# Kernel tuning notes

Hardware: AMD Instinct MI355X
Metric: run time of the kernel (lower is better)

Reference implementation:

```python
import jax, jax.numpy as jnp
import numpy as np

N = 4096      # num_nodes (also node feature dim)
E = 32768     # num_edges
EMB = 8       # embedding_dim


def setup_inputs() -> dict:
    key = jax.random.key(0)
    ks = jax.random.split(key, 12)
    s = lambda fan_in: 1.0 / np.sqrt(fan_in)
    return {
        "x": jax.random.normal(ks[0], (N, N), dtype=jnp.float32),
        "edge_index": jax.random.randint(ks[1], (2, E), 0, N, dtype=jnp.int64),
        "edge_weight": jax.random.uniform(ks[2], (E,), dtype=jnp.float32),
        # GCNConv linear (PyG Linear, weight [out,in]) + bias
        "gcn_w": jax.random.normal(ks[3], (N, N), dtype=jnp.float32) * s(N),
        "gcn_b": jnp.zeros((N,), dtype=jnp.float32),
        # Wq: Linear(N -> E)
        "wq_w": jax.random.normal(ks[4], (E, N), dtype=jnp.float32) * s(N),
        "wq_b": jax.random.normal(ks[5], (E,), dtype=jnp.float32) * s(N),
        # edge embedding table [E, EMB]
        "emb": jax.random.normal(ks[6], (E, EMB), dtype=jnp.float32),
        # WF: Linear(N+EMB -> 1)
        "wf_w": jax.random.normal(ks[7], (1, N + EMB), dtype=jnp.float32) * s(N + EMB),
        "wf_b": jax.random.normal(ks[8], (1,), dtype=jnp.float32) * s(N + EMB),
    }


def reference(x, edge_index, edge_weight, gcn_w, gcn_b, wq_w, wq_b, emb, wf_w, wf_b):
    n = x.shape[0]
    row, col = edge_index[0], edge_index[1]
    # --- GCNConv: add self loops (weight 1.0), symmetric normalization ---
    loop = jnp.arange(n)
    row_f = jnp.concatenate([row, loop])
    col_f = jnp.concatenate([col, loop])
    w_f = jnp.concatenate([edge_weight, jnp.ones((n,), dtype=x.dtype)])
    deg = jax.ops.segment_sum(w_f, col_f, num_segments=n)          # weighted in-degree
    dis = jnp.where(deg > 0, jax.lax.rsqrt(deg), 0.0)              # deg^{-1/2}, 0 for isolated
    norm = dis[row_f] * w_f * dis[col_f]                           # [E+N]
    h = x @ gcn_w.T                                                # linear transform first (as PyG)
    agg = jax.ops.segment_sum(norm[:, None] * h[row_f], col_f, num_segments=n)
    H1 = jnp.tanh(agg + gcn_b)                                     # [N, N]
    # --- dense head ---
    H2 = jnp.tanh(H1 @ wq_w.T + wq_b)                              # [N, E]
    H2_t = H2.T                                                    # [E, N]
    feat = jnp.concatenate([H2_t, emb], axis=1)                    # [E, N+EMB]
    F_hat = (feat @ wf_w.T + wf_b)[:, 0]                           # [E]
    return F_hat
```

## Files before the change

kernel.cpp:

```cpp
#include <hip/hip_runtime.h>
#include <hip/hip_bf16.h>

#define NN 4096
#define NE 32768
#define NEMB 8

typedef __bf16 bf16x8 __attribute__((ext_vector_type(8)));
typedef float  f32x4  __attribute__((ext_vector_type(4)));

__device__ __forceinline__ unsigned short f2bf(float f) {
  union { float f; unsigned int u; } v; v.f = f;
  return (unsigned short)((v.u + 0x7FFFu + ((v.u >> 16) & 1u)) >> 16);
}

__global__ void k_f2bf(const float* __restrict__ in, unsigned short* __restrict__ out, long n8) {
  long i = (long)blockIdx.x * blockDim.x + threadIdx.x;
  long stride = (long)gridDim.x * blockDim.x;
  for (long j = i; j < n8; j += stride) {
    const float* p = in + j * 8;
    float4 a = *(const float4*)p;
    float4 b = *(const float4*)(p + 4);
    union { unsigned short u[8]; uint4 v; } o;
    o.u[0] = f2bf(a.x); o.u[1] = f2bf(a.y); o.u[2] = f2bf(a.z); o.u[3] = f2bf(a.w);
    o.u[4] = f2bf(b.x); o.u[5] = f2bf(b.y); o.u[6] = f2bf(b.z); o.u[7] = f2bf(b.w);
    *(uint4*)(out + j * 8) = o.v;
  }
}

__global__ void k_deg_init(float* deg) { deg[blockIdx.x * 256 + threadIdx.x] = 1.0f; }

__global__ void k_edge_accum(const int* __restrict__ ei, const float* __restrict__ ew,
                             float* deg, int* cnt) {
  int e = blockIdx.x * 256 + threadIdx.x;
  if (e >= NE) return;
  int c = ei[NE + e];
  atomicAdd(&deg[c], ew[e]);
  atomicAdd(&cnt[c], 1);
}

__global__ void k_dis(const float* __restrict__ deg, float* __restrict__ dis) {
  int i = blockIdx.x * 256 + threadIdx.x;
  float d = deg[i];
  dis[i] = d > 0.f ? rsqrtf(d) : 0.f;
}

__global__ void k_scan(const int* __restrict__ cnt, int* __restrict__ starts) {
  __shared__ int sh[1024];
  int tid = threadIdx.x;
  int base = tid * 4;
  int v[4]; int sum = 0;
  for (int i = 0; i < 4; i++) { v[i] = cnt[base + i]; sum += v[i]; }
  sh[tid] = sum;
  __syncthreads();
  for (int offd = 1; offd < 1024; offd <<= 1) {
    int t = (tid >= offd) ? sh[tid - offd] : 0;
    __syncthreads();
    sh[tid] += t;
    __syncthreads();
  }
  int run = sh[tid] - sum;
  for (int i = 0; i < 4; i++) { starts[base + i] = run; run += v[i]; }
}

__global__ void k_fill(const int* __restrict__ ei, const int* __restrict__ starts,
                       int* cursor, int* csr_e) {
  int e = blockIdx.x * 256 + threadIdx.x;
  if (e >= NE) return;
  int c = ei[NE + e];
  int pos = atomicAdd(&cursor[c], 1);
  csr_e[starts[c] + pos] = e;
}

__global__ void k_sortnorm(const int* __restrict__ ei, const float* __restrict__ ew,
                           const int* __restrict__ starts, const int* __restrict__ cnt,
                           const float* __restrict__ dis,
                           int* csr_e, int* __restrict__ csr_row, float* __restrict__ csr_nrm) {
  int n = blockIdx.x * 256 + threadIdx.x;
  if (n >= NN) return;
  int s = starts[n], c = cnt[n];
  for (int i = 1; i < c; i++) {
    int key = csr_e[s + i]; int j = i - 1;
    while (j >= 0 && csr_e[s + j] > key) { csr_e[s + j + 1] = csr_e[s + j]; j--; }
    csr_e[s + j + 1] = key;
  }
  float dn = dis[n];
  for (int i = 0; i < c; i++) {
    int e = csr_e[s + i];
    int r = ei[e];
    csr_row[s + i] = r;
    csr_nrm[s + i] = dis[r] * ew[e] * dn;
  }
}

__global__ __launch_bounds__(256) void k_agg(
    const float* __restrict__ h, const float* __restrict__ dis,
    const int* __restrict__ starts, const int* __restrict__ cnt,
    const int* __restrict__ csr_row, const float* __restrict__ csr_nrm,
    const float* __restrict__ gcn_b, unsigned short* __restrict__ H1b) {
  int n = blockIdx.x;
  int tid = threadIdx.x;
  float dn = dis[n];
  float sw = dn * dn;
  float acc[16];
  const float* hn = h + (size_t)n * NN;
  #pragma unroll
  for (int i = 0; i < 16; i++) { int f = tid + i * 256; acc[i] = sw * hn[f] + gcn_b[f]; }
  int s = starts[n], c = cnt[n];
  __shared__ int   s_row[64];
  __shared__ float s_nrm[64];
  for (int base = 0; base < c; base += 64) {
    int m = min(64, c - base);
    __syncthreads();
    if (tid < m) { s_row[tid] = csr_row[s + base + tid]; s_nrm[tid] = csr_nrm[s + base + tid]; }
    __syncthreads();
    for (int j = 0; j < m; j++) {
      const float* hr = h + (size_t)s_row[j] * NN;
      float wgt = s_nrm[j];
      #pragma unroll
      for (int i = 0; i < 16; i++) acc[i] += wgt * hr[tid + i * 256];
    }
  }
  #pragma unroll
  for (int i = 0; i < 16; i++)
    H1b[(size_t)n * NN + tid + i * 256] = f2bf(tanhf(acc[i]));
}

__device__ __forceinline__ void gload16(const void* g, void* l) {
  __builtin_amdgcn_global_load_lds(
      (const __attribute__((address_space(1))) unsigned int*)g,
      (__attribute__((address_space(3))) unsigned int*)l, 16, 0, 0);
}

#define BARX() do { __builtin_amdgcn_sched_barrier(0); __builtin_amdgcn_s_barrier(); __builtin_amdgcn_sched_barrier(0); } while (0)
#define VMC(n) do { asm volatile("s_waitcnt vmcnt(" #n ")" ::: "memory"); } while (0)


#define STAGE(buf, mat, kk, tk) do { \
    size_t off_ = (size_t)(tk) * 64 + (kk) * 32; \
    gload16((mat ? gB0 : gA0) + off_, &LDS[buf][mat][kk][c0][0]); \
    gload16((mat ? gB1 : gA1) + off_, &LDS[buf][mat][kk][c0 + 1][0]); \
  } while (0)

#define LDA4(dst, buf, kk, q) do { \
    const unsigned short* b_ = &LDS[buf][0][kk][wr * 8 + (q) * 4][0] + aoff; \
    dst[0] = *(const bf16x8*)(b_); \
    dst[1] = *(const bf16x8*)(b_ + 512); \
    dst[2] = *(const bf16x8*)(b_ + 1024); \
    dst[3] = *(const bf16x8*)(b_ + 1536); \
  } while (0)

#define LDB4(dst, buf, kk) do { \
    const unsigned short* b_ = &LDS[buf][1][kk][wc * 4][0] + aoff; \
    dst[0] = *(const bf16x8*)(b_); \
    dst[1] = *(const bf16x8*)(b_ + 512); \
    dst[2] = *(const bf16x8*)(b_ + 1024); \
    dst[3] = *(const bf16x8*)(b_ + 1536); \
  } while (0)

#define MMA16(q, av, bv) do { \
    __builtin_amdgcn_s_setprio(1); \
    _Pragma("unroll") \
    for (int mf_ = 0; mf_ < 4; mf_++) \
      _Pragma("unroll") \
      for (int nf_ = 0; nf_ < 4; nf_++) \
        acc[(q) * 4 + mf_][nf_] = __builtin_amdgcn_mfma_f32_16x16x32_bf16(av[mf_], bv[nf_], acc[(q) * 4 + mf_][nf_], 0, 0, 0); \
    __builtin_amdgcn_s_setprio(0); \
  } while (0)

template<bool FUSED>
__global__ __launch_bounds__(512, 2) void gemm8(
    const unsigned short* __restrict__ A,
    const unsigned short* __restrict__ B,
    int N, int K, int nRb,
    float* __restrict__ outF,
    const float* __restrict__ colBias,
    const float* __restrict__ rowW,
    float* __restrict__ P) {
  __shared__ unsigned short LDS[2][2][2][16][512];

  const int nwg = gridDim.x, n8 = nwg >> 3;
  const int bid = blockIdx.x;
  const int swz = (bid & 7) * n8 + (bid >> 3);
  const int rb = swz % nRb, cb = swz / nRb;
  const int row0 = rb * 256, col0 = cb * 256;

  const int tid = threadIdx.x;
  const int w = tid >> 6, l = tid & 63;
  const int wr = w >> 2, wc = w & 3;
  const int l15 = l & 15, kl = l >> 4;

  const int c0 = w * 2;
  const int pq = l >> 2;
  const int pc = (l & 3) ^ ((l >> 3) & 3);
  const unsigned short* gA0 = A + (size_t)(row0 + c0 * 16 + pq) * K + pc * 8;
  const unsigned short* gA1 = gA0 + (size_t)16 * K;
  const unsigned short* gB0 = B + (size_t)(col0 + c0 * 16 + pq) * K + pc * 8;
  const unsigned short* gB1 = gB0 + (size_t)16 * K;

  const int aoff = l15 * 32 + ((kl ^ ((l >> 1) & 3)) << 3);

  f32x4 acc[8][4];
  #pragma unroll
  for (int m = 0; m < 8; m++)
    #pragma unroll
    for (int n = 0; n < 4; n++)
      acc[m][n] = f32x4{0.f, 0.f, 0.f, 0.f};

  STAGE(0, 0, 0, 0); STAGE(0, 1, 0, 0); STAGE(0, 0, 1, 0); STAGE(0, 1, 1, 0);
  STAGE(1, 0, 0, 1); STAGE(1, 1, 0, 1);
  VMC(4);
  BARX();

  const int NIT = K >> 7;
  for (int i = 0; i < NIT; i++) {
    const int ta = 2 * i, tb = 2 * i + 1;
    const bool mid = (i < NIT - 1);
    bf16x8 av[4], bv[4];
    LDB4(bv, 0, 0); LDA4(av, 0, 0, 0);
    STAGE(1, 0, 1, tb);
    MMA16(0, av, bv);
    BARX();
    LDA4(av, 0, 0, 1);
    STAGE(1, 1, 1, tb);
    MMA16(1, av, bv);
    VMC(8);
    BARX();
    LDB4(bv, 0, 1); LDA4(av, 0, 1, 0);
    if (mid) STAGE(0, 0, 0, ta + 2);
    MMA16(0, av, bv);
    BARX();
    LDA4(av, 0, 1, 1);
    if (mid) STAGE(0, 1, 0, ta + 2);
    MMA16(1, av, bv);
    if (mid) VMC(8); else VMC(4);
    BARX();
    LDB4(bv, 1, 0); LDA4(av, 1, 0, 0);
    if (mid) STAGE(0, 0, 1, ta + 2);
    MMA16(0, av, bv);
    BARX();
    LDA4(av, 1, 0, 1);
    if (mid) STAGE(0, 1, 1, ta + 2);
    MMA16(1, av, bv);
    if (mid) VMC(8); else VMC(0);
    BARX();
    LDB4(bv, 1, 1); LDA4(av, 1, 1, 0);
    if (mid) STAGE(1, 0, 0, tb + 2);
    MMA16(0, av, bv);
    BARX();
    LDA4(av, 1, 1, 1);
    if (mid) STAGE(1, 1, 0, tb + 2);
    MMA16(1, av, bv);
    if (mid) VMC(8);
    BARX();
  }

  if (!FUSED) {
    #pragma unroll
    for (int mf = 0; mf < 8; mf++)
      #pragma unroll
      for (int nf = 0; nf < 4; nf++) {
        int row = row0 + wr * 128 + mf * 16 + kl * 4;
        int col = col0 + wc * 64 + nf * 16 + l15;
        float* o = outF + (size_t)row * N + col;
        #pragma unroll
        for (int r = 0; r < 4; r++) o[(size_t)r * N] = acc[mf][nf][r];
      }
  } else {
    #pragma unroll
    for (int nf = 0; nf < 4; nf++) {
      int col = col0 + wc * 64 + nf * 16 + l15;
      float bias = colBias[col];
      float s = 0.f;
      #pragma unroll
      for (int mf = 0; mf < 8; mf++) {
        int rbase = row0 + wr * 128 + mf * 16 + kl * 4;
        #pragma unroll
        for (int r = 0; r < 4; r++)
          s += rowW[rbase + r] * tanhf(acc[mf][nf][r] + bias);
      }
      s += __shfl_xor(s, 16, 64);
      s += __shfl_xor(s, 32, 64);
      if (l < 16) P[(size_t)(rb * 2 + wr) * N + col] = s;
    }
  }
}

__global__ void k_final(const float* __restrict__ P, const float* __restrict__ emb,
                        const float* __restrict__ wf, const float* __restrict__ wfb,
                        float* __restrict__ out) {
  int e = blockIdx.x * 256 + threadIdx.x;
  float s = 0.f;
  for (int r = 0; r < 32; r++) s += P[(size_t)r * NE + e];
  float c = wfb[0];
  #pragma unroll
  for (int k = 0; k < NEMB; k++) c += emb[e * NEMB + k] * wf[NN + k];
  out[e] = s + c;
}

extern "C" void kernel_launch(void* const* d_in, const int* in_sizes, int n_in,
                              void* d_out, int out_size, void* d_ws, size_t ws_size,
                              hipStream_t stream) {
  const float* x    = (const float*)d_in[0];
  const int*   ei   = (const int*)d_in[1];
  const float* ew   = (const float*)d_in[2];
  const float* gcnw = (const float*)d_in[3];
  const float* gcnb = (const float*)d_in[4];
  const float* wqw  = (const float*)d_in[5];
  const float* wqb  = (const float*)d_in[6];
  const float* emb  = (const float*)d_in[7];
  const float* wfw  = (const float*)d_in[8];
  const float* wfb  = (const float*)d_in[9];
  float* out = (float*)d_out;

  char* ws = (char*)d_ws;
  size_t off = 0;
  auto alloc = [&](size_t b) { char* p = ws + off; off += (b + 255) & ~(size_t)255; return p; };

  unsigned short* wq16  = (unsigned short*)alloc((size_t)NE * NN * 2);
  float*          h     = (float*)alloc((size_t)NN * NN * 4);
  unsigned short* x16   = (unsigned short*)alloc((size_t)NN * NN * 2);
  unsigned short* w16   = (unsigned short*)alloc((size_t)NN * NN * 2);
  unsigned short* h1b   = (unsigned short*)alloc((size_t)NN * NN * 2);
  float* deg    = (float*)alloc(NN * 4);
  float* dis    = (float*)alloc(NN * 4);
  int*   cnt    = (int*)alloc(NN * 4);
  int*   cursor = (int*)alloc(NN * 4);
  int*   starts = (int*)alloc(NN * 4);
  int*   csr_e  = (int*)alloc(NE * 4);
  int*   csr_row= (int*)alloc(NE * 4);
  float* csr_nrm= (float*)alloc(NE * 4);
  float* P      = (float*)alloc((size_t)32 * NE * 4);

  hipMemsetAsync(cnt, 0, NN * 4 * 2, stream);

  k_deg_init<<<NN / 256, 256, 0, stream>>>(deg);
  k_edge_accum<<<NE / 256, 256, 0, stream>>>(ei, ew, deg, cnt);
  k_dis<<<NN / 256, 256, 0, stream>>>(deg, dis);
  k_scan<<<1, 1024, 0, stream>>>(cnt, starts);
  k_fill<<<NE / 256, 256, 0, stream>>>(ei, starts, cursor, csr_e);
  k_sortnorm<<<NN / 256, 256, 0, stream>>>(ei, ew, starts, cnt, dis, csr_e, csr_row, csr_nrm);

  k_f2bf<<<1024, 256, 0, stream>>>(x, x16, (long)NN * NN / 8);
  k_f2bf<<<1024, 256, 0, stream>>>(gcnw, w16, (long)NN * NN / 8);
  k_f2bf<<<2048, 256, 0, stream>>>(wqw, wq16, (long)NE * NN / 8);

  gemm8<false><<<16 * 16, 512, 0, stream>>>(x16, w16, NN, NN, 16, h, nullptr, nullptr, nullptr);

  k_agg<<<NN, 256, 0, stream>>>(h, dis, starts, cnt, csr_row, csr_nrm, gcnb, h1b);

  gemm8<true><<<16 * 128, 512, 0, stream>>>(h1b, wq16, NE, NN, 16, nullptr, wqb, wfw, P);

  k_final<<<NE / 256, 256, 0, stream>>>(P, emb, wfw, wfb, out);
}
```

Measured before the change: 1.416 ms.

## Store GCN linear output as bf16 and interleave A-fragment LDS reads with MFMAs

The intermediate h = x @ gcn_w.T is now written and read as bf16 instead of fp32. This halves the store traffic of the first GEMM and the gather traffic in the aggregation kernel. The GEMM main loop is also restructured so the next A fragments are read from LDS inside the MFMA loop, software-pipelining LDS reads behind matrix ops, with a trailing MMA after the loop. The cost is reduced precision of h and more intricate register and barrier sequencing.

```diff
diff --git a/kernel.cpp b/kernel.cpp
--- a/kernel.cpp
+++ b/kernel.cpp
@@ -11,6 +11,10 @@
 __device__ __forceinline__ unsigned short f2bf(float f) {
   union { float f; unsigned int u; } v; v.f = f;
   return (unsigned short)((v.u + 0x7FFFu + ((v.u >> 16) & 1u)) >> 16);
+}
+__device__ __forceinline__ float b2f(unsigned short u) {
+  union { unsigned int u; float f; } v; v.u = ((unsigned int)u) << 16;
+  return v.f;
 }
 
 __global__ void k_f2bf(const float* __restrict__ in, unsigned short* __restrict__ out, long n8) {
@@ -93,7 +97,7 @@
 }
 
 __global__ __launch_bounds__(256) void k_agg(
-    const float* __restrict__ h, const float* __restrict__ dis,
+    const unsigned short* __restrict__ h, const float* __restrict__ dis,
     const int* __restrict__ starts, const int* __restrict__ cnt,
     const int* __restrict__ csr_row, const float* __restrict__ csr_nrm,
     const float* __restrict__ gcn_b, unsigned short* __restrict__ H1b) {
@@ -102,9 +106,9 @@
   float dn = dis[n];
   float sw = dn * dn;
   float acc[16];
-  const float* hn = h + (size_t)n * NN;
+  const unsigned short* hn = h + (size_t)n * NN;
   #pragma unroll
-  for (int i = 0; i < 16; i++) { int f = tid + i * 256; acc[i] = sw * hn[f] + gcn_b[f]; }
+  for (int i = 0; i < 16; i++) { int f = tid + i * 256; acc[i] = sw * b2f(hn[f]) + gcn_b[f]; }
   int s = starts[n], c = cnt[n];
   __shared__ int   s_row[64];
   __shared__ float s_nrm[64];
@@ -114,10 +118,10 @@
     if (tid < m) { s_row[tid] = csr_row[s + base + tid]; s_nrm[tid] = csr_nrm[s + base + tid]; }
     __syncthreads();
     for (int j = 0; j < m; j++) {
-      const float* hr = h + (size_t)s_row[j] * NN;
+      const unsigned short* hr = h + (size_t)s_row[j] * NN;
       float wgt = s_nrm[j];
       #pragma unroll
-      for (int i = 0; i < 16; i++) acc[i] += wgt * hr[tid + i * 256];
+      for (int i = 0; i < 16; i++) acc[i] += wgt * b2f(hr[tid + i * 256]);
     }
   }
   #pragma unroll
@@ -157,7 +161,20 @@
     dst[3] = *(const bf16x8*)(b_ + 1536); \
   } while (0)
 
-#define MMA16(q, av, bv) do { \
+#define MMA_RDA(q, bufA, kkA, qA) do { \
+    __builtin_amdgcn_s_setprio(1); \
+    _Pragma("unroll") \
+    for (int mf_ = 0; mf_ < 4; mf_++) { \
+      _Pragma("unroll") \
+      for (int nf_ = 0; nf_ < 4; nf_++) \
+        acc[(q) * 4 + mf_][nf_] = __builtin_amdgcn_mfma_f32_16x16x32_bf16(av[mf_], bv[nf_], acc[(q) * 4 + mf_][nf_], 0, 0, 0); \
+      const unsigned short* a_ = &LDS[bufA][0][kkA][wr * 8 + (qA) * 4 + mf_][0] + aoff; \
+      av[mf_] = *(const bf16x8*)(a_); \
+    } \
+    __builtin_amdgcn_s_setprio(0); \
+  } while (0)
+
+#define MMA16(q) do { \
     __builtin_amdgcn_s_setprio(1); \
     _Pragma("unroll") \
     for (int mf_ = 0; mf_ < 4; mf_++) \
@@ -172,7 +189,7 @@
     const unsigned short* __restrict__ A,
     const unsigned short* __restrict__ B,
     int N, int K, int nRb,
-    float* __restrict__ outF,
+    void* __restrict__ outP,
     const float* __restrict__ colBias,
     const float* __restrict__ rowW,
     float* __restrict__ P) {
@@ -206,6 +223,8 @@
     for (int n = 0; n < 4; n++)
       acc[m][n] = f32x4{0.f, 0.f, 0.f, 0.f};
 
+  bf16x8 av[4], bv[4];
+
   STAGE(0, 0, 0, 0); STAGE(0, 1, 0, 0); STAGE(0, 0, 1, 0); STAGE(0, 1, 1, 0);
   STAGE(1, 0, 0, 1); STAGE(1, 1, 0, 1);
   VMC(4);
@@ -215,55 +234,57 @@
   for (int i = 0; i < NIT; i++) {
     const int ta = 2 * i, tb = 2 * i + 1;
     const bool mid = (i < NIT - 1);
-    bf16x8 av[4], bv[4];
-    LDB4(bv, 0, 0); LDA4(av, 0, 0, 0);
+    if (i) {
+      MMA_RDA(1, 0, 0, 0);
+      LDB4(bv, 0, 0);
+    } else {
+      LDA4(av, 0, 0, 0);
+      LDB4(bv, 0, 0);
+    }
     STAGE(1, 0, 1, tb);
-    MMA16(0, av, bv);
-    BARX();
-    LDA4(av, 0, 0, 1);
+    BARX();
+    MMA_RDA(0, 0, 0, 1);
     STAGE(1, 1, 1, tb);
-    MMA16(1, av, bv);
     VMC(8);
     BARX();
-    LDB4(bv, 0, 1); LDA4(av, 0, 1, 0);
+    MMA_RDA(1, 0, 1, 0);
+    LDB4(bv, 0, 1);
     if (mid) STAGE(0, 0, 0, ta + 2);
-    MMA16(0, av, bv);
-    BARX();
-    LDA4(av, 0, 1, 1);
+    BARX();
+    MMA_RDA(0, 0, 1, 1);
     if (mid) STAGE(0, 1, 0, ta + 2);
-    MMA16(1, av, bv);
     if (mid) VMC(8); else VMC(4);
     BARX();
-    LDB4(bv, 1, 0); LDA4(av, 1, 0, 0);
+    MMA_RDA(1, 1, 0, 0);
+    LDB4(bv, 1, 0);
     if (mid) STAGE(0, 0, 1, ta + 2);
-    MMA16(0, av, bv);
-    BARX();
-    LDA4(av, 1, 0, 1);
+    BARX();
+    MMA_RDA(0, 1, 0, 1);
     if (mid) STAGE(0, 1, 1, ta + 2);
-    MMA16(1, av, bv);
     if (mid) VMC(8); else VMC(0);
     BARX();
-    LDB4(bv, 1, 1); LDA4(av, 1, 1, 0);
+    MMA_RDA(1, 1, 1, 0);
+    LDB4(bv, 1, 1);
     if (mid) STAGE(1, 0, 0, tb + 2);
-    MMA16(0, av, bv);
-    BARX();
-    LDA4(av, 1, 1, 1);
+    BARX();
+    MMA_RDA(0, 1, 1, 1);
     if (mid) STAGE(1, 1, 0, tb + 2);
-    MMA16(1, av, bv);
     if (mid) VMC(8);
     BARX();
   }
+  MMA16(1);
 
   if (!FUSED) {
+    unsigned short* outB = (unsigned short*)outP;
     #pragma unroll
     for (int mf = 0; mf < 8; mf++)
       #pragma unroll
       for (int nf = 0; nf < 4; nf++) {
         int row = row0 + wr * 128 + mf * 16 + kl * 4;
         int col = col0 + wc * 64 + nf * 16 + l15;
-        float* o = outF + (size_t)row * N + col;
+        unsigned short* o = outB + (size_t)row * N + col;
         #pragma unroll
-        for (int r = 0; r < 4; r++) o[(size_t)r * N] = acc[mf][nf][r];
+        for (int r = 0; r < 4; r++) o[(size_t)r * N] = f2bf(acc[mf][nf][r]);
       }
   } else {
     #pragma unroll
@@ -317,7 +338,7 @@
   auto alloc = [&](size_t b) { char* p = ws + off; off += (b + 255) & ~(size_t)255; return p; };
 
   unsigned short* wq16  = (unsigned short*)alloc((size_t)NE * NN * 2);
-  float*          h     = (float*)alloc((size_t)NN * NN * 4);
+  unsigned short* h     = (unsigned short*)alloc((size_t)NN * NN * 2);
   unsigned short* x16   = (unsigned short*)alloc((size_t)NN * NN * 2);
   unsigned short* w16   = (unsigned short*)alloc((size_t)NN * NN * 2);
   unsigned short* h1b   = (unsigned short*)alloc((size_t)NN * NN * 2);
```

New measurement: 1.365 ms, median of 2. 3.6% less time.
